# Performance work log

Hardware: AMD Instinct MI355X
Metric: run time of the kernel (lower is better)

The kernel has to match this reference:

```python
import jax, jax.numpy as jnp
import numpy as np

B, S, N, BS, D, H, V = 1, 2048, 128, 16, 512, 8, 32000
MASK_TOKEN_ID = 3


def setup_inputs() -> dict:
    key = jax.random.key(0)
    ks = jax.random.split(key, 10)
    anchors = jnp.sort(jax.random.randint(ks[0], (B, N), 0, S - BS), axis=1)
    return {
        "input_ids": jax.random.randint(ks[1], (B, S), 0, V),
        "hidden_states": jax.random.normal(ks[2], (B, S, D), dtype=jnp.float32),
        "loss_mask": jnp.ones((B, S), dtype=jnp.float32),
        "anchor_positions": anchors,
        "block_keep_mask": jnp.ones((B, N), dtype=bool),
        "embed_table": jax.random.normal(ks[3], (V, D), dtype=jnp.float32) * 0.02,
        "Wq": jax.random.normal(ks[4], (D, D), dtype=jnp.float32) * 0.02,
        "Wk": jax.random.normal(ks[5], (D, D), dtype=jnp.float32) * 0.02,
        "Wv": jax.random.normal(ks[6], (D, D), dtype=jnp.float32) * 0.02,
        "Wo": jax.random.normal(ks[7], (D, D), dtype=jnp.float32) * 0.02,
        "W_lm": jax.random.normal(ks[8], (D, V), dtype=jnp.float32) * 0.02,
    }


def dflash_sdpa_mask(anchor_positions, block_keep_mask):
    # KV layout: [context S | block_0 .. block_{N-1}], Q layout: [block_0 .. block_{N-1}]
    Q = N * BS
    KV = S + N * BS
    q_idx = jnp.arange(Q)              # [Q]
    kv_idx = jnp.arange(KV)            # [KV]
    q_blk = q_idx // BS                # [Q]
    anchor_q = anchor_positions[:, q_blk]          # [B,Q] anchor of each query's block
    keep_q = block_keep_mask[:, q_blk]             # [B,Q]
    is_ctx = kv_idx < S                             # [KV]
    mask_context = is_ctx[None, None, :] & (kv_idx[None, None, :] < anchor_q[:, :, None])  # [B,Q,KV]
    kv_blk = (kv_idx - S) // BS
    mask_draft = (kv_idx >= S)[None, :] & (q_blk[:, None] == kv_blk[None, :])              # [Q,KV]
    final = (mask_context | mask_draft[None]) & keep_q[:, :, None]                          # [B,Q,KV]
    return final


def reference(input_ids, hidden_states, loss_mask, anchor_positions, block_keep_mask,
              embed_table, Wq, Wk, Wv, Wo, W_lm):
    dh = D // H
    Q = N * BS

    # --- noise embedding: MASK token everywhere, anchor token at each block start ---
    safe_anchor = jnp.clip(anchor_positions, 0, S - 1)                     # [B,N]
    anchor_tokens = jnp.take_along_axis(input_ids, safe_anchor, axis=1)    # [B,N]
    start_tokens = jnp.where(block_keep_mask, anchor_tokens, MASK_TOKEN_ID)
    noise_ids = jnp.full((B, Q), MASK_TOKEN_ID, dtype=input_ids.dtype)
    noise_ids = noise_ids.at[:, jnp.arange(N) * BS].set(start_tokens)
    noise_embedding = embed_table[noise_ids]                               # [B,Q,D]

    # --- draft attention: Q = draft tokens, KV = [context hiddens | draft tokens] ---
    kv_in = jnp.concatenate([hidden_states, noise_embedding], axis=1)      # [B,S+Q,D]
    q = (noise_embedding @ Wq).reshape(B, Q, H, dh)
    k = (kv_in @ Wk).reshape(B, S + Q, H, dh)
    v = (kv_in @ Wv).reshape(B, S + Q, H, dh)
    scores = jnp.einsum("bqhd,bkhd->bhqk", q, k) / jnp.sqrt(jnp.float32(dh))
    mask = dflash_sdpa_mask(anchor_positions, block_keep_mask)[:, None]    # [B,1,Q,KV]
    attn = jax.nn.softmax(jnp.where(mask, scores, -1e9), axis=-1)
    out = jnp.einsum("bhqk,bkhd->bqhd", attn, v).reshape(B, Q, D) @ Wo     # [B,Q,D]
    logits = out @ W_lm                                                    # [B,Q,V]

    # --- block-wise CE loss ---
    offs = jnp.arange(BS)
    label_idx = anchor_positions[:, :, None] + offs[None, None, :]         # [B,N,BS]
    valid_label = label_idx < S
    safe_idx = jnp.clip(label_idx, 0, S - 1)
    ids_b = jnp.broadcast_to(input_ids[:, None, :], (B, N, S))
    target_ids = jnp.take_along_axis(ids_b, safe_idx, axis=2)              # [B,N,BS]
    lm_b = jnp.broadcast_to(loss_mask[:, None, :], (B, N, S))
    lm_g = jnp.take_along_axis(lm_b, safe_idx, axis=2)
    weight = (block_keep_mask[:, :, None].astype(jnp.float32)
              * valid_label.astype(jnp.float32)
              * (offs > 0)[None, None, :].astype(jnp.float32)
              * lm_g)                                                      # [B,N,BS]

    flat_logits = logits.reshape(-1, V)
    flat_targets = target_ids.reshape(-1)
    flat_w = weight.reshape(-1)
    logp = jax.nn.log_softmax(flat_logits, axis=-1)
    loss_per = -jnp.take_along_axis(logp, flat_targets[:, None], axis=1)[:, 0]
    loss = jnp.sum(loss_per * flat_w) / (jnp.sum(flat_w) + 1e-6)

    pred = jnp.argmax(flat_logits, axis=-1)
    correct = (pred == flat_targets) & (flat_w > 0.5)
    accuracy = jnp.sum(correct).astype(jnp.float32) / (jnp.sum(flat_w) + 1e-6)
    return loss, accuracy
```

## Files before the change

### kernel.cpp

```cpp
#include <hip/hip_runtime.h>

typedef unsigned short u16;
typedef __attribute__((ext_vector_type(4))) float f32x4;
typedef __attribute__((ext_vector_type(8))) short short8;
typedef __attribute__((ext_vector_type(4))) unsigned int uv4;
typedef __attribute__((ext_vector_type(4))) float fv4;
typedef __attribute__((ext_vector_type(4))) unsigned short usv4;

#define S_LEN 2048
#define NBLK 128
#define DMODEL 512
#define VOCAB 32000
#define QLEN 2048
#define KVLEN 4096
#define NSPLIT 250

#define GAS(p) ((const __attribute__((address_space(1))) void*)(const void*)(p))
#define LAS(p) ((__attribute__((address_space(3))) void*)(void*)(p))

__device__ __forceinline__ float bf2f(u16 u){
  union { unsigned int i; float f; } x; x.i = ((unsigned int)u) << 16; return x.f;
}
__device__ __forceinline__ u16 f2bf(float f){
  union { float f; unsigned int i; } x; x.f = f;
  unsigned int r = x.i + 0x7fffu + ((x.i >> 16) & 1u);
  return (u16)(r >> 16);
}

__global__ __launch_bounds__(256) void prep_w(const float* __restrict__ Wq, const float* __restrict__ Wk,
                                              const float* __restrict__ Wv, const float* __restrict__ Wo,
                                              const float* __restrict__ Wlm,
                                              u16* __restrict__ WqT, u16* __restrict__ WkT,
                                              u16* __restrict__ WvT, u16* __restrict__ WoT,
                                              u16* __restrict__ Wf){
  __shared__ float tile[64][33];
  int t = threadIdx.x;
  int id = blockIdx.x;
  if (id < 1024){
    const float* in; u16* out;
    switch (id >> 8){
      case 0: in = Wq; out = WqT; break;
      case 1: in = Wk; out = WkT; break;
      case 2: in = Wv; out = WvT; break;
      default: in = Wo; out = WoT; break;
    }
    int rem = id & 255;
    int nb = (rem & 15) * 32, kb = (rem >> 4) * 32;
    int tx = t & 31, ty = t >> 5;
    #pragma unroll
    for (int i = 0; i < 4; i++){
      int r = ty + i * 8;
      tile[r][tx] = in[(size_t)(kb + r) * 512 + nb + tx];
    }
    __syncthreads();
    #pragma unroll
    for (int i = 0; i < 4; i++){
      int r = ty + i * 8;
      out[(size_t)(nb + r) * 512 + kb + tx] = f2bf(tile[tx][r]);
    }
  } else {
    int j = id - 1024;
    int vb32 = j % 1000, kblk = j / 1000;
    int tx = t & 31, ty = t >> 5;
    #pragma unroll
    for (int i = 0; i < 8; i++){
      int r = ty + i * 8;
      tile[r][tx] = Wlm[(size_t)(kblk * 64 + r) * VOCAB + vb32 * 32 + tx];
    }
    __syncthreads();
    int w = t >> 6, lane = t & 63;
    int v16sel = w & 1, ktsel = w >> 1;
    int gsel = lane >> 4, li = lane & 15;
    u16 tmp[8];
    #pragma unroll
    for (int jj = 0; jj < 8; jj++)
      tmp[jj] = f2bf(tile[ktsel * 32 + gsel * 8 + jj][v16sel * 16 + li]);
    size_t v16 = vb32 * 2 + v16sel;
    size_t kt32 = kblk * 2 + ktsel;
    *(uv4*)&Wf[((v16 * 16 + kt32) * 64 + lane) * 8] = *(uv4*)tmp;
  }
}

__global__ __launch_bounds__(128) void build_kv(const float* __restrict__ hidden,
                                                const float* __restrict__ embed,
                                                const int* __restrict__ input_ids,
                                                const int* __restrict__ anchors,
                                                const unsigned char* __restrict__ keep,
                                                u16* __restrict__ kvb){
  int row = blockIdx.x;
  int t = threadIdx.x;
  const float* src;
  if (row < S_LEN){
    src = hidden + (size_t)row * DMODEL;
  } else {
    int q = row - S_LEN;
    int id = 3;
    if ((q & 15) == 0){
      int n = q >> 4;
      if (keep[n]){
        int a = anchors[n]; a = min(max(a, 0), S_LEN - 1);
        id = input_ids[a];
      }
    }
    src = embed + (size_t)id * DMODEL;
  }
  int c = t * 4;
  fv4 v = *(const fv4*)&src[c];
  usv4 o; o[0] = f2bf(v[0]); o[1] = f2bf(v[1]); o[2] = f2bf(v[2]); o[3] = f2bf(v[3]);
  *(usv4*)&kvb[(size_t)row * DMODEL + c] = o;
}

__global__ __launch_bounds__(256) void qkv_gemm(const u16* __restrict__ kvb,
                                                const u16* __restrict__ WkT,
                                                const u16* __restrict__ WvT,
                                                const u16* __restrict__ WqT,
                                                u16* __restrict__ kb,
                                                u16* __restrict__ vTb,
                                                u16* __restrict__ qb2){
  __shared__ __align__(16) u16 As[2][128 * 64];
  __shared__ __align__(16) u16 Bs[2][64 * 64];
  int id = blockIdx.x;
  const u16* A = kvb; const u16* BT; u16* C; int ldc; int trans = 0;
  int rowbase, colbase;
  if (id < 256){
    BT = WkT; C = kb; ldc = 512;
    rowbase = (id & 31) * 128; colbase = (id >> 5) * 64;
  } else if (id < 512){
    int j = id - 256;
    BT = WvT; C = vTb; ldc = KVLEN; trans = 1;
    rowbase = (j & 31) * 128; colbase = (j >> 5) * 64;
  } else {
    int j = id - 512;
    A = kvb + (size_t)S_LEN * DMODEL;
    BT = WqT; C = qb2; ldc = 512;
    rowbase = (j & 15) * 128; colbase = (j >> 4) * 64;
  }
  int t = threadIdx.x, w = t >> 6, lane = t & 63;
  int g = lane >> 4, li = lane & 15;
  int r0 = t >> 3, cg0 = t & 7;
  int swz = (cg0 ^ (r0 & 7)) << 3;

  auto stageA = [&](u16* dst, int kb_){
    #pragma unroll
    for (int i = 0; i < 4; i++)
      __builtin_amdgcn_global_load_lds(GAS(&A[(size_t)(rowbase + r0 + i * 32) * DMODEL + kb_ + swz]),
                                       LAS(dst + i * 2048 + w * 512), 16, 0, 0);
  };
  auto stageB = [&](u16* dst, int kb_){
    #pragma unroll
    for (int i = 0; i < 2; i++)
      __builtin_amdgcn_global_load_lds(GAS(&BT[(size_t)(colbase + r0 + i * 32) * DMODEL + kb_ + swz]),
                                       LAS(dst + i * 2048 + w * 512), 16, 0, 0);
  };

  f32x4 acc[2][4];
  #pragma unroll
  for (int i = 0; i < 2; i++)
    #pragma unroll
    for (int j = 0; j < 4; j++)
      acc[i][j] = (f32x4){0.f, 0.f, 0.f, 0.f};

  stageA(As[0], 0); stageB(Bs[0], 0);

  for (int kt = 0; kt < 8; kt++){
    u16* curA = As[kt & 1]; u16* curB = Bs[kt & 1];
    if (kt < 7){
      stageA(As[(kt + 1) & 1], (kt + 1) * 64); stageB(Bs[(kt + 1) & 1], (kt + 1) * 64);
      asm volatile("s_waitcnt vmcnt(6)" ::: "memory");
    } else {
      asm volatile("s_waitcnt vmcnt(0)" ::: "memory");
    }
    __builtin_amdgcn_s_barrier();
    #pragma unroll
    for (int ks = 0; ks < 2; ks++){
      short8 af[2], bf[4];
      #pragma unroll
      for (int mf = 0; mf < 2; mf++){
        int row = w * 32 + mf * 16 + li;
        af[mf] = *(const short8*)&curA[row * 64 + (((ks * 4 + g) ^ (li & 7)) << 3)];
      }
      #pragma unroll
      for (int nf = 0; nf < 4; nf++){
        int row = nf * 16 + li;
        bf[nf] = *(const short8*)&curB[row * 64 + (((ks * 4 + g) ^ (li & 7)) << 3)];
      }
      #pragma unroll
      for (int mf = 0; mf < 2; mf++)
        #pragma unroll
        for (int nf = 0; nf < 4; nf++)
          acc[mf][nf] = __builtin_amdgcn_mfma_f32_16x16x32_bf16(af[mf], bf[nf], acc[mf][nf], 0, 0, 0);
    }
    __builtin_amdgcn_s_barrier();
  }

  #pragma unroll
  for (int mf = 0; mf < 2; mf++)
    #pragma unroll
    for (int nf = 0; nf < 4; nf++)
      #pragma unroll
      for (int r = 0; r < 4; r++){
        int row = rowbase + w * 32 + mf * 16 + g * 4 + r;
        int col = colbase + nf * 16 + li;
        u16 vv = f2bf(acc[mf][nf][r]);
        if (trans) C[(size_t)col * ldc + row] = vv;
        else       C[(size_t)row * ldc + col] = vv;
      }
}

__global__ __launch_bounds__(256) void gemmO(const u16* __restrict__ A,
                                             const u16* __restrict__ BT,
                                             u16* __restrict__ C){
  __shared__ __align__(16) u16 As[2][128 * 64];
  __shared__ __align__(16) u16 Bs[2][64 * 64];
  int t = threadIdx.x, w = t >> 6, lane = t & 63;
  int g = lane >> 4, li = lane & 15;
  int rowbase = blockIdx.x * 128, colbase = blockIdx.y * 64;
  int r0 = t >> 3, cg0 = t & 7;
  int swz = (cg0 ^ (r0 & 7)) << 3;

  auto stageA = [&](u16* dst, int kb_){
    #pragma unroll
    for (int i = 0; i < 4; i++)
      __builtin_amdgcn_global_load_lds(GAS(&A[(size_t)(rowbase + r0 + i * 32) * DMODEL + kb_ + swz]),
                                       LAS(dst + i * 2048 + w * 512), 16, 0, 0);
  };
  auto stageB = [&](u16* dst, int kb_){
    #pragma unroll
    for (int i = 0; i < 2; i++)
      __builtin_amdgcn_global_load_lds(GAS(&BT[(size_t)(colbase + r0 + i * 32) * DMODEL + kb_ + swz]),
                                       LAS(dst + i * 2048 + w * 512), 16, 0, 0);
  };

  f32x4 acc[2][4];
  #pragma unroll
  for (int i = 0; i < 2; i++)
    #pragma unroll
    for (int j = 0; j < 4; j++)
      acc[i][j] = (f32x4){0.f, 0.f, 0.f, 0.f};

  stageA(As[0], 0); stageB(Bs[0], 0);

  for (int kt = 0; kt < 8; kt++){
    u16* curA = As[kt & 1]; u16* curB = Bs[kt & 1];
    if (kt < 7){
      stageA(As[(kt + 1) & 1], (kt + 1) * 64); stageB(Bs[(kt + 1) & 1], (kt + 1) * 64);
      asm volatile("s_waitcnt vmcnt(6)" ::: "memory");
    } else {
      asm volatile("s_waitcnt vmcnt(0)" ::: "memory");
    }
    __builtin_amdgcn_s_barrier();
    #pragma unroll
    for (int ks = 0; ks < 2; ks++){
      short8 af[2], bf[4];
      #pragma unroll
      for (int mf = 0; mf < 2; mf++){
        int row = w * 32 + mf * 16 + li;
        af[mf] = *(const short8*)&curA[row * 64 + (((ks * 4 + g) ^ (li & 7)) << 3)];
      }
      #pragma unroll
      for (int nf = 0; nf < 4; nf++){
        int row = nf * 16 + li;
        bf[nf] = *(const short8*)&curB[row * 64 + (((ks * 4 + g) ^ (li & 7)) << 3)];
      }
      #pragma unroll
      for (int mf = 0; mf < 2; mf++)
        #pragma unroll
        for (int nf = 0; nf < 4; nf++)
          acc[mf][nf] = __builtin_amdgcn_mfma_f32_16x16x32_bf16(af[mf], bf[nf], acc[mf][nf], 0, 0, 0);
    }
    __builtin_amdgcn_s_barrier();
  }

  #pragma unroll
  for (int mf = 0; mf < 2; mf++)
    #pragma unroll
    for (int nf = 0; nf < 4; nf++)
      #pragma unroll
      for (int r = 0; r < 4; r++){
        int row = rowbase + w * 32 + mf * 16 + g * 4 + r;
        int col = colbase + nf * 16 + li;
        C[(size_t)row * DMODEL + col] = f2bf(acc[mf][nf][r]);
      }
}

__global__ __launch_bounds__(256) void attn_mfma(const u16* __restrict__ qb,
                                                 const u16* __restrict__ kb,
                                                 const u16* __restrict__ vT,
                                                 const int* __restrict__ anchors,
                                                 const unsigned char* __restrict__ keep,
                                                 u16* __restrict__ attnb){
  int bx = blockIdx.x;
  int n = (bx & 1) ? (NBLK - 1 - (bx >> 1)) : (bx >> 1);
  int h = blockIdx.y;
  int t = threadIdx.x, w = t >> 6, lane = t & 63;
  int g = lane >> 4, li = lane & 15;

  __shared__ __align__(16) u16 q_s[16][72];
  __shared__ __align__(16) u16 p_s[4][16][72];
  __shared__ float o_s[4][16][64];
  __shared__ float l_s[4][16];

  {
    int r = t >> 4, c4 = (t & 15) * 4;
    usv4 v = *(const usv4*)&qb[(size_t)(n * 16 + r) * DMODEL + h * 64 + c4];
    usv4 o;
    #pragma unroll
    for (int j = 0; j < 4; j++) o[j] = f2bf(bf2f(v[j]) * 0.125f);
    *(usv4*)&q_s[r][c4] = o;
  }
  __syncthreads();

  int anchor = anchors[n];
  bool kp = keep[n] != 0;
  const u16* kh  = kb + h * 64;
  const u16* vTh = vT + (size_t)(h * 64) * KVLEN;

  if (!kp){
    if (w == 0){
      float acc = 0.f;
      const u16* row = vTh + (size_t)lane * KVLEN;
      for (int k2 = 0; k2 < KVLEN; k2 += 8){
        short8 vv = *(const short8*)&row[k2];
        #pragma unroll
        for (int j = 0; j < 8; j++) acc += bf2f((u16)vv[j]);
      }
      acc *= (1.f / 4096.f);
      u16 ov = f2bf(acc);
      for (int r = 0; r < 16; r++)
        attnb[(size_t)(n * 16 + r) * DMODEL + h * 64 + lane] = ov;
    }
    return;
  }

  short8 qa[2];
  #pragma unroll
  for (int ks = 0; ks < 2; ks++)
    qa[ks] = *(const short8*)&q_s[li][ks * 32 + g * 8];

  int nctx = (anchor + 63) >> 6;
  int ntot = nctx + 1;

  f32x4 o_acc[4];
  float l[4];
  #pragma unroll
  for (int i = 0; i < 4; i++){ o_acc[i] = (f32x4){0.f,0.f,0.f,0.f}; l[i] = 0.f; }

  for (int c = w; c < ntot; c += 4){
    bool draft = (c == nctx);
    int kbase = draft ? (S_LEN + n * 16) : c * 64;
    int nk    = draft ? 16 : min(64, anchor - c * 64);

    f32x4 s[4];
    #pragma unroll
    for (int nf = 0; nf < 4; nf++) s[nf] = (f32x4){0.f,0.f,0.f,0.f};
    #pragma unroll
    for (int ks = 0; ks < 2; ks++){
      #pragma unroll
      for (int nf = 0; nf < 4; nf++){
        int krow = min(kbase + nf * 16 + li, KVLEN - 1);
        short8 bfrag = *(const short8*)&kh[(size_t)krow * DMODEL + ks * 32 + g * 8];
        s[nf] = __builtin_amdgcn_mfma_f32_16x16x32_bf16(qa[ks], bfrag, s[nf], 0, 0, 0);
      }
    }

    #pragma unroll
    for (int r = 0; r < 4; r++){
      float ps = 0.f;
      #pragma unroll
      for (int nf = 0; nf < 4; nf++){
        float p = (nf * 16 + li < nk) ? __expf(s[nf][r]) : 0.f;
        ps += p;
        p_s[w][g * 4 + r][nf * 16 + li] = f2bf(p);
      }
      #pragma unroll
      for (int mm = 1; mm < 16; mm <<= 1) ps += __shfl_xor(ps, mm);
      l[r] += ps;
    }

    #pragma unroll
    for (int ks = 0; ks < 2; ks++){
      short8 pa = *(const short8*)&p_s[w][li][ks * 32 + g * 8];
      int kcol = min(kbase + ks * 32 + g * 8, KVLEN - 8);
      #pragma unroll
      for (int nfd = 0; nfd < 4; nfd++){
        short8 vfrag = *(const short8*)&vTh[(size_t)(nfd * 16 + li) * KVLEN + kcol];
        o_acc[nfd] = __builtin_amdgcn_mfma_f32_16x16x32_bf16(pa, vfrag, o_acc[nfd], 0, 0, 0);
      }
    }
  }

  #pragma unroll
  for (int r = 0; r < 4; r++){
    if (li == 0) l_s[w][g * 4 + r] = l[r];
    #pragma unroll
    for (int nfd = 0; nfd < 4; nfd++)
      o_s[w][g * 4 + r][nfd * 16 + li] = o_acc[nfd][r];
  }
  __syncthreads();

  {
    int row = t >> 4, c0 = (t & 15) * 4;
    float L = l_s[0][row] + l_s[1][row] + l_s[2][row] + l_s[3][row];
    float inv = 1.f / L;
    #pragma unroll
    for (int j = 0; j < 4; j++){
      float ov = o_s[0][row][c0 + j] + o_s[1][row][c0 + j] + o_s[2][row][c0 + j] + o_s[3][row][c0 + j];
      attnb[(size_t)(n * 16 + row) * DMODEL + h * 64 + c0 + j] = f2bf(ov * inv);
    }
  }
}

__global__ __launch_bounds__(256) void lm_fused(const u16* __restrict__ obp,
                                                const u16* __restrict__ Wf,
                                                const int* __restrict__ input_ids,
                                                const int* __restrict__ anchors,
                                                float* __restrict__ pl,
                                                float* __restrict__ pt, float* __restrict__ pbv,
                                                int* __restrict__ pbi){
  __shared__ __align__(16) u16 Ob[2][128 * 64];
  __shared__ int tcol_s[128];

  int L = blockIdx.x;
  int T = (L & 7) * 500 + (L >> 3);
  int qbase = (T & 15) * 128;
  int vb = T >> 4;
  int vocabbase = vb * 128;
  int t = threadIdx.x, w = t >> 6, lane = t & 63;
  int g = lane >> 4, li = lane & 15;
  int wv = w & 1, wq = w >> 1;

  if (t < 128){
    int r = qbase + t; int n = r >> 4, off = r & 15;
    int lab = anchors[n] + off;
    int safe = min(max(lab, 0), S_LEN - 1);
    tcol_s[t] = input_ids[safe];
  }

  int r0 = t >> 3, cg0 = t & 7;
  int swz = (cg0 ^ (r0 & 7)) << 3;
  auto stageO = [&](u16* odst, int kt){
    #pragma unroll
    for (int i = 0; i < 4; i++)
      __builtin_amdgcn_global_load_lds(GAS(&obp[(size_t)(qbase + r0 + i * 32) * DMODEL + kt * 64 + swz]),
                                       LAS(odst + i * 2048 + w * 512), 16, 0, 0);
  };
  const u16* wbase = Wf + ((size_t)(vb * 8 + wv * 4) * 16) * 512 + lane * 8;

  f32x4 acc[4][4];
  #pragma unroll
  for (int i = 0; i < 4; i++)
    #pragma unroll
    for (int j = 0; j < 4; j++)
      acc[i][j] = (f32x4){0.f, 0.f, 0.f, 0.f};

  stageO(Ob[0], 0);

  for (int kt = 0; kt < 8; kt++){
    const u16* curO = Ob[kt & 1];
    short8 wfr[2][4];
    if (kt < 7){
      stageO(Ob[(kt + 1) & 1], kt + 1);
      #pragma unroll
      for (int ks = 0; ks < 2; ks++)
        #pragma unroll
        for (int vf = 0; vf < 4; vf++)
          wfr[ks][vf] = *(const short8*)(wbase + ((size_t)(vf * 16 + kt * 2 + ks) * 64) * 8);
      asm volatile("s_waitcnt vmcnt(12)" ::: "memory");
    } else {
      #pragma unroll
      for (int ks = 0; ks < 2; ks++)
        #pragma unroll
        for (int vf = 0; vf < 4; vf++)
          wfr[ks][vf] = *(const short8*)(wbase + ((size_t)(vf * 16 + kt * 2 + ks) * 64) * 8);
      asm volatile("s_waitcnt vmcnt(8)" ::: "memory");
    }
    __builtin_amdgcn_s_barrier();
    __builtin_amdgcn_s_setprio(1);
    #pragma unroll
    for (int ks = 0; ks < 2; ks++){
      short8 obf[4];
      #pragma unroll
      for (int qf = 0; qf < 4; qf++)
        obf[qf] = *(const short8*)&curO[(wq * 64 + qf * 16 + li) * 64 + (((ks * 4 + g) ^ (li & 7)) << 3)];
      #pragma unroll
      for (int vf = 0; vf < 4; vf++)
        #pragma unroll
        for (int qf = 0; qf < 4; qf++)
          acc[vf][qf] = __builtin_amdgcn_mfma_f32_16x16x32_bf16(wfr[ks][vf], obf[qf], acc[vf][qf], 0, 0, 0);
    }
    __builtin_amdgcn_s_setprio(0);
    __builtin_amdgcn_s_barrier();
  }
  __syncthreads();

  float* cse = (float*)&Ob[0][0];
  float* ctv = (float*)&Ob[0][512];
  float* cbv = (float*)&Ob[0][1024];
  int*   cbi = (int*)  &Ob[0][1536];

  #pragma unroll
  for (int qf = 0; qf < 4; qf++){
    int qloc = wq * 64 + qf * 16 + li;
    int tc = tcol_s[qloc] - (vocabbase + wv * 64);
    float se = 0.f, tv = -3e38f, bv = -3e38f; int bi = 0x7fffffff;
    #pragma unroll
    for (int vf = 0; vf < 4; vf++){
      #pragma unroll
      for (int r = 0; r < 4; r++){
        float v = acc[vf][qf][r];
        int pos = vf * 16 + g * 4 + r;
        se += __expf(v);
        if (pos == tc) tv = v;
        if (v > bv){ bv = v; bi = pos; }
      }
    }
    #pragma unroll
    for (int off = 16; off <= 32; off <<= 1){
      se += __shfl_xor(se, off);
      tv = fmaxf(tv, __shfl_xor(tv, off));
      float ob_ = __shfl_xor(bv, off); int oi = __shfl_xor(bi, off);
      if (ob_ > bv || (ob_ == bv && oi < bi)){ bv = ob_; bi = oi; }
    }
    if (g == 0){
      cse[wv * 128 + qloc] = se; ctv[wv * 128 + qloc] = tv;
      cbv[wv * 128 + qloc] = bv; cbi[wv * 128 + qloc] = wv * 64 + bi;
    }
  }
  __syncthreads();

  if (t < 128){
    float SE = 0.f, TV = -3e38f, BV = -3e38f; int BI = 0x7fffffff;
    #pragma unroll
    for (int vv = 0; vv < 2; vv++){
      SE += cse[vv * 128 + t];
      TV = fmaxf(TV, ctv[vv * 128 + t]);
      float v = cbv[vv * 128 + t];
      if (v > BV){ BV = v; BI = cbi[vv * 128 + t]; }
    }
    size_t idx = (size_t)vb * QLEN + qbase + t;
    pl[idx] = SE; pt[idx] = TV; pbv[idx] = BV; pbi[idx] = vocabbase + BI;
  }
}

__global__ __launch_bounds__(256) void loss_rows(const float* __restrict__ pl,
                                                 const float* __restrict__ pt, const float* __restrict__ pbv,
                                                 const int* __restrict__ pbi,
                                                 const int* __restrict__ input_ids,
                                                 const int* __restrict__ anchors,
                                                 const unsigned char* __restrict__ keep,
                                                 const float* __restrict__ loss_mask,
                                                 float* __restrict__ rowacc){
  int t = threadIdx.x, w = t >> 6, lane = t & 63;
  int row = blockIdx.x * 4 + w;
  float L = 0.f, TV = -3e38f, BV = -3e38f; int BI = 0x7fffffff;
  for (int s = lane; s < NSPLIT; s += 64){
    size_t idx = (size_t)s * QLEN + row;
    L += pl[idx];
    TV = fmaxf(TV, pt[idx]);
    float bv_ = pbv[idx]; int bi_ = pbi[idx];
    if (bv_ > BV || (bv_ == BV && bi_ < BI)){ BV = bv_; BI = bi_; }
  }
  #pragma unroll
  for (int mm = 1; mm < 64; mm <<= 1){
    L += __shfl_xor(L, mm);
    TV = fmaxf(TV, __shfl_xor(TV, mm));
    float ob = __shfl_xor(BV, mm); int oi = __shfl_xor(BI, mm);
    if (ob > BV || (ob == BV && oi < BI)){ BV = ob; BI = oi; }
  }
  if (lane == 0){
    int n = row >> 4, off = row & 15;
    int lab = anchors[n] + off;
    int valid = (lab < S_LEN) ? 1 : 0;
    int safe = min(max(lab, 0), S_LEN - 1);
    int tgt = input_ids[safe];
    float wgt = (keep[n] ? 1.f : 0.f) * (valid ? 1.f : 0.f) * ((off > 0) ? 1.f : 0.f) * loss_mask[safe];
    float logp = TV - __logf(L);
    rowacc[row * 3 + 0] = -logp * wgt;
    rowacc[row * 3 + 1] = wgt;
    rowacc[row * 3 + 2] = ((BI == tgt) && (wgt > 0.5f)) ? 1.f : 0.f;
  }
}

__global__ __launch_bounds__(256) void final_sum(const float* __restrict__ rowacc, float* __restrict__ out){
  int t = threadIdx.x;
  float a = 0.f, b = 0.f, c = 0.f;
  for (int r = t; r < QLEN; r += 256){
    a += rowacc[r * 3 + 0]; b += rowacc[r * 3 + 1]; c += rowacc[r * 3 + 2];
  }
  __shared__ float sa[256], sb[256], sc_[256];
  sa[t] = a; sb[t] = b; sc_[t] = c;
  __syncthreads();
  for (int s = 128; s >= 1; s >>= 1){
    if (t < s){ sa[t] += sa[t + s]; sb[t] += sb[t + s]; sc_[t] += sc_[t + s]; }
    __syncthreads();
  }
  if (t == 0){
    out[0] = sa[0] / (sb[0] + 1e-6f);
    out[1] = sc_[0] / (sb[0] + 1e-6f);
  }
}

extern "C" void kernel_launch(void* const* d_in, const int* in_sizes, int n_in,
                              void* d_out, int out_size, void* d_ws, size_t ws_size,
                              hipStream_t stream) {
  const int*   input_ids = (const int*)  d_in[0];
  const float* hidden    = (const float*)d_in[1];
  const float* loss_mask = (const float*)d_in[2];
  const int*   anchors   = (const int*)  d_in[3];
  const unsigned char* keep = (const unsigned char*)d_in[4];
  const float* embed     = (const float*)d_in[5];
  const float* Wq        = (const float*)d_in[6];
  const float* Wk        = (const float*)d_in[7];
  const float* Wv        = (const float*)d_in[8];
  const float* Wo        = (const float*)d_in[9];
  const float* Wlm       = (const float*)d_in[10];

  char* ws = (char*)d_ws;
  size_t off = 0;
  auto take = [&](size_t bytes) -> char* {
    char* p = ws + off;
    off += (bytes + 255) & ~(size_t)255;
    return p;
  };
  u16* WqT  = (u16*)take((size_t)512 * 512 * 2);
  u16* WkT  = (u16*)take((size_t)512 * 512 * 2);
  u16* WvT  = (u16*)take((size_t)512 * 512 * 2);
  u16* WoT  = (u16*)take((size_t)512 * 512 * 2);
  u16* Wfrag= (u16*)take((size_t)VOCAB * 512 * 2);
  u16* kvb  = (u16*)take((size_t)KVLEN * 512 * 2);
  u16* qb2  = (u16*)take((size_t)QLEN * 512 * 2);
  u16* kb   = (u16*)take((size_t)KVLEN * 512 * 2);
  u16* vTb  = (u16*)take((size_t)512 * KVLEN * 2);
  u16* attnb= (u16*)take((size_t)QLEN * 512 * 2);
  u16* ob   = (u16*)take((size_t)QLEN * 512 * 2);
  float* pl = (float*)take((size_t)QLEN * NSPLIT * 4);
  float* pt = (float*)take((size_t)QLEN * NSPLIT * 4);
  float* pbv= (float*)take((size_t)QLEN * NSPLIT * 4);
  int*   pbi= (int*)  take((size_t)QLEN * NSPLIT * 4);
  float* rowacc = (float*)take((size_t)QLEN * 3 * 4);

  prep_w<<<9024, 256, 0, stream>>>(Wq, Wk, Wv, Wo, Wlm, WqT, WkT, WvT, WoT, Wfrag);

  build_kv<<<KVLEN, 128, 0, stream>>>(hidden, embed, input_ids, anchors, keep, kvb);

  qkv_gemm<<<640, 256, 0, stream>>>(kvb, WkT, WvT, WqT, kb, vTb, qb2);

  attn_mfma<<<dim3(NBLK, 8), 256, 0, stream>>>(qb2, kb, vTb, anchors, keep, attnb);

  gemmO<<<dim3(16, 8), 256, 0, stream>>>(attnb, WoT, ob);

  lm_fused<<<4000, 256, 0, stream>>>(ob, Wfrag, input_ids, anchors, pl, pt, pbv, pbi);

  loss_rows<<<512, 256, 0, stream>>>(pl, pt, pbv, pbi, input_ids, anchors, keep, loss_mask, rowacc);

  final_sum<<<1, 256, 0, stream>>>(rowacc, (float*)d_out);
}
```

Baseline: 200.8 us.

## Pre-fragment LM-head activations and load MFMA operands directly from global

Result: slower. 213.5 us (+6.3%).

```diff
diff --git a/kernel.cpp b/kernel.cpp
--- a/kernel.cpp
+++ b/kernel.cpp
@@ -283,6 +283,14 @@
       }
 }
 
+__global__ __launch_bounds__(256) void ob_frag(const u16* __restrict__ ob, u16* __restrict__ Of){
+  int id = blockIdx.x * 4 + (threadIdx.x >> 6);
+  int q16 = id >> 4, kt32 = id & 15;
+  int lane = threadIdx.x & 63, g = lane >> 4, li = lane & 15;
+  short8 v = *(const short8*)&ob[(size_t)(q16 * 16 + li) * DMODEL + kt32 * 32 + g * 8];
+  *(short8*)&Of[((size_t)(q16 * 16 + kt32) * 64 + lane) * 8] = v;
+}
+
 __global__ __launch_bounds__(256) void attn_mfma(const u16* __restrict__ qb,
                                                  const u16* __restrict__ kb,
                                                  const u16* __restrict__ vT,
@@ -410,20 +418,22 @@
   }
 }
 
-__global__ __launch_bounds__(256) void lm_fused(const u16* __restrict__ obp,
+__global__ __launch_bounds__(256) void lm_fused(const u16* __restrict__ Of,
                                                 const u16* __restrict__ Wf,
                                                 const int* __restrict__ input_ids,
                                                 const int* __restrict__ anchors,
                                                 float* __restrict__ pl,
                                                 float* __restrict__ pt, float* __restrict__ pbv,
                                                 int* __restrict__ pbi){
-  __shared__ __align__(16) u16 Ob[2][128 * 64];
   __shared__ int tcol_s[128];
+  __shared__ float cse[2][128], ctv[2][128], cbv[2][128];
+  __shared__ int cbi[2][128];
 
   int L = blockIdx.x;
   int T = (L & 7) * 500 + (L >> 3);
-  int qbase = (T & 15) * 128;
+  int qblk = T & 15;
   int vb = T >> 4;
+  int qbase = qblk * 128;
   int vocabbase = vb * 128;
   int t = threadIdx.x, w = t >> 6, lane = t & 63;
   int g = lane >> 4, li = lane & 15;
@@ -436,15 +446,8 @@
     tcol_s[t] = input_ids[safe];
   }
 
-  int r0 = t >> 3, cg0 = t & 7;
-  int swz = (cg0 ^ (r0 & 7)) << 3;
-  auto stageO = [&](u16* odst, int kt){
-    #pragma unroll
-    for (int i = 0; i < 4; i++)
-      __builtin_amdgcn_global_load_lds(GAS(&obp[(size_t)(qbase + r0 + i * 32) * DMODEL + kt * 64 + swz]),
-                                       LAS(odst + i * 2048 + w * 512), 16, 0, 0);
-  };
-  const u16* wbase = Wf + ((size_t)(vb * 8 + wv * 4) * 16) * 512 + lane * 8;
+  const u16* wbase = Wf + (size_t)(vb * 8 + wv * 4) * 8192 + lane * 8;
+  const u16* obase = Of + (size_t)(qblk * 8 + wq * 4) * 8192 + lane * 8;
 
   f32x4 acc[4][4];
   #pragma unroll
@@ -453,50 +456,20 @@
     for (int j = 0; j < 4; j++)
       acc[i][j] = (f32x4){0.f, 0.f, 0.f, 0.f};
 
-  stageO(Ob[0], 0);
-
-  for (int kt = 0; kt < 8; kt++){
-    const u16* curO = Ob[kt & 1];
-    short8 wfr[2][4];
-    if (kt < 7){
-      stageO(Ob[(kt + 1) & 1], kt + 1);
-      #pragma unroll
-      for (int ks = 0; ks < 2; ks++)
-        #pragma unroll
-        for (int vf = 0; vf < 4; vf++)
-          wfr[ks][vf] = *(const short8*)(wbase + ((size_t)(vf * 16 + kt * 2 + ks) * 64) * 8);
-      asm volatile("s_waitcnt vmcnt(12)" ::: "memory");
-    } else {
-      #pragma unroll
-      for (int ks = 0; ks < 2; ks++)
-        #pragma unroll
-        for (int vf = 0; vf < 4; vf++)
-          wfr[ks][vf] = *(const short8*)(wbase + ((size_t)(vf * 16 + kt * 2 + ks) * 64) * 8);
-      asm volatile("s_waitcnt vmcnt(8)" ::: "memory");
-    }
-    __builtin_amdgcn_s_barrier();
-    __builtin_amdgcn_s_setprio(1);
-    #pragma unroll
-    for (int ks = 0; ks < 2; ks++){
-      short8 obf[4];
+  for (int kt = 0; kt < 16; kt++){
+    short8 wfr[4], obf[4];
+    #pragma unroll
+    for (int vf = 0; vf < 4; vf++)
+      wfr[vf] = *(const short8*)(wbase + (size_t)vf * 8192 + kt * 512);
+    #pragma unroll
+    for (int qf = 0; qf < 4; qf++)
+      obf[qf] = *(const short8*)(obase + (size_t)qf * 8192 + kt * 512);
+    #pragma unroll
+    for (int vf = 0; vf < 4; vf++)
       #pragma unroll
       for (int qf = 0; qf < 4; qf++)
-        obf[qf] = *(const short8*)&curO[(wq * 64 + qf * 16 + li) * 64 + (((ks * 4 + g) ^ (li & 7)) << 3)];
-      #pragma unroll
-      for (int vf = 0; vf < 4; vf++)
-        #pragma unroll
-        for (int qf = 0; qf < 4; qf++)
-          acc[vf][qf] = __builtin_amdgcn_mfma_f32_16x16x32_bf16(wfr[ks][vf], obf[qf], acc[vf][qf], 0, 0, 0);
-    }
-    __builtin_amdgcn_s_setprio(0);
-    __builtin_amdgcn_s_barrier();
-  }
-  __syncthreads();
-
-  float* cse = (float*)&Ob[0][0];
-  float* ctv = (float*)&Ob[0][512];
-  float* cbv = (float*)&Ob[0][1024];
-  int*   cbi = (int*)  &Ob[0][1536];
+        acc[vf][qf] = __builtin_amdgcn_mfma_f32_16x16x32_bf16(wfr[vf], obf[qf], acc[vf][qf], 0, 0, 0);
+  }
 
   #pragma unroll
   for (int qf = 0; qf < 4; qf++){
@@ -522,8 +495,8 @@
       if (ob_ > bv || (ob_ == bv && oi < bi)){ bv = ob_; bi = oi; }
     }
     if (g == 0){
-      cse[wv * 128 + qloc] = se; ctv[wv * 128 + qloc] = tv;
-      cbv[wv * 128 + qloc] = bv; cbi[wv * 128 + qloc] = wv * 64 + bi;
+      cse[wv][qloc] = se; ctv[wv][qloc] = tv;
+      cbv[wv][qloc] = bv; cbi[wv][qloc] = wv * 64 + bi;
     }
   }
   __syncthreads();
@@ -532,10 +505,10 @@
     float SE = 0.f, TV = -3e38f, BV = -3e38f; int BI = 0x7fffffff;
     #pragma unroll
     for (int vv = 0; vv < 2; vv++){
-      SE += cse[vv * 128 + t];
-      TV = fmaxf(TV, ctv[vv * 128 + t]);
-      float v = cbv[vv * 128 + t];
-      if (v > BV){ BV = v; BI = cbi[vv * 128 + t]; }
+      SE += cse[vv][t];
+      TV = fmaxf(TV, ctv[vv][t]);
+      float v = cbv[vv][t];
+      if (v > BV){ BV = v; BI = cbi[vv][t]; }
     }
     size_t idx = (size_t)vb * QLEN + qbase + t;
     pl[idx] = SE; pt[idx] = TV; pbv[idx] = BV; pbi[idx] = vocabbase + BI;
@@ -633,6 +606,7 @@
   u16* vTb  = (u16*)take((size_t)512 * KVLEN * 2);
   u16* attnb= (u16*)take((size_t)QLEN * 512 * 2);
   u16* ob   = (u16*)take((size_t)QLEN * 512 * 2);
+  u16* Ofrag= (u16*)take((size_t)QLEN * 512 * 2);
   float* pl = (float*)take((size_t)QLEN * NSPLIT * 4);
   float* pt = (float*)take((size_t)QLEN * NSPLIT * 4);
   float* pbv= (float*)take((size_t)QLEN * NSPLIT * 4);
@@ -649,7 +623,9 @@
 
   gemmO<<<dim3(16, 8), 256, 0, stream>>>(attnb, WoT, ob);
 
-  lm_fused<<<4000, 256, 0, stream>>>(ob, Wfrag, input_ids, anchors, pl, pt, pbv, pbi);
+  ob_frag<<<512, 256, 0, stream>>>(ob, Ofrag);
+
+  lm_fused<<<4000, 256, 0, stream>>>(Ofrag, Wfrag, input_ids, anchors, pl, pt, pbv, pbi);
 
   loss_rows<<<512, 256, 0, stream>>>(pl, pt, pbv, pbi, input_ids, anchors, keep, loss_mask, rowacc);
 
```
